# Kernel optimization log

Measured on AMD Instinct MI355X. Metric: run time of the kernel, lower is better.

Reference implementation:

```python
import jax, jax.numpy as jnp
import numpy as np

N, E, DIN, DOUT = 50000, 500000, 128, 128


def setup_inputs() -> dict:
    key = jax.random.key(0)
    ks = jax.random.split(key, 12)
    s = 0.02
    return {
        "x": jax.random.normal(ks[0], (N, DIN), jnp.float32),
        "pos": jax.random.normal(ks[1], (N, 3), jnp.float32),
        "edge_index": jax.random.randint(ks[2], (2, E), 0, N, jnp.int64),
        # mlp_h: Linear(DIN,DIN) -> ReLU -> Linear(DIN,3) -> Tanh
        "h_w1": jax.random.normal(ks[3], (DIN, DIN), jnp.float32) * s,
        "h_b1": jnp.zeros((DIN,), jnp.float32),
        "h_w2": jax.random.normal(ks[4], (DIN, 3), jnp.float32) * s,
        "h_b2": jnp.zeros((3,), jnp.float32),
        # mlp_f: Linear(DIN+3, DOUT) -> ReLU
        "f_w": jax.random.normal(ks[5], (DIN + 3, DOUT), jnp.float32) * s,
        "f_b": jnp.zeros((DOUT,), jnp.float32),
        # mlp_g: Linear(DOUT,DOUT) -> ReLU -> Linear(DOUT,DIN) -> ReLU
        "g_w1": jax.random.normal(ks[6], (DOUT, DOUT), jnp.float32) * s,
        "g_b1": jnp.zeros((DOUT,), jnp.float32),
        "g_w2": jax.random.normal(ks[7], (DOUT, DIN), jnp.float32) * s,
        "g_b2": jnp.zeros((DIN,), jnp.float32),
    }


def reference(x, pos, edge_index, h_w1, h_b1, h_w2, h_b2, f_w, f_b,
              g_w1, g_b1, g_w2, g_b2):
    # PointGNNConv (aggr='sum'):
    #   delta = mlp_h(x)                                   [N, 3]
    #   msg_e = mlp_f([pos_j - pos_i + delta_i, x_j])      [E, DOUT]
    #   agg_i = sum_{j in N(i)} msg_e                       [N, DOUT]
    #   out   = x + mlp_g(agg)                              [N, DIN]
    delta = jnp.tanh(jax.nn.relu(x @ h_w1 + h_b1) @ h_w2 + h_b2)
    src = edge_index[0]  # j (source)
    dst = edge_index[1]  # i (target)
    edge_feat = jnp.concatenate(
        [pos[src] - pos[dst] + delta[dst], x[src]], axis=-1)  # [E, DIN+3]
    msg = jax.nn.relu(edge_feat @ f_w + f_b)                   # [E, DOUT]
    agg = jax.ops.segment_sum(msg, dst, num_segments=N)        # [N, DOUT]
    out = jax.nn.relu(jax.nn.relu(agg @ g_w1 + g_b1) @ g_w2 + g_b2)
    return x + out
```

## Files before the change

### kernel.cpp

```cpp
#include <hip/hip_runtime.h>
#include <hip/hip_bf16.h>

typedef float f32x4 __attribute__((ext_vector_type(4)));
typedef short bf16x8 __attribute__((ext_vector_type(8)));
typedef unsigned short u16x8 __attribute__((ext_vector_type(8)));

#define MFMA16(a, b, c) __builtin_amdgcn_mfma_f32_16x16x32_bf16((a), (b), (c), 0, 0, 0)
#define BCAP 128

static __device__ __forceinline__ short f2bf(float f) {
    union { float f; unsigned u; } v; v.f = f;
    unsigned r = v.u + 0x7FFFu + ((v.u >> 16) & 1u);
    return (short)(r >> 16);
}
static __device__ __forceinline__ float bflo(unsigned u) {
    union { unsigned u; float f; } v; v.u = u << 16; return v.f;
}
static __device__ __forceinline__ float bfhi(unsigned u) {
    union { unsigned u; float f; } v; v.u = u & 0xffff0000u; return v.f;
}
static __device__ __forceinline__ unsigned packbf(float lo, float hi) {
    return ((unsigned)(unsigned short)f2bf(lo)) | (((unsigned)(unsigned short)f2bf(hi)) << 16);
}

__global__ __launch_bounds__(256) void k_prep(
    const float* __restrict__ hw1, const float* __restrict__ fw,
    const float* __restrict__ gw1, const float* __restrict__ gw2,
    unsigned short* __restrict__ wT,
    const int* __restrict__ ei, int* __restrict__ flag,
    int* __restrict__ cursor, int N)
{
    const int gtid = blockIdx.x * 256 + threadIdx.x;
    if (gtid == 0) {
        int nz = 0;
        for (int i = 0; i < 64; ++i) nz |= ei[2 * i + 1];
        *flag = (nz != 0) ? 1 : 0;
    }
    for (int i = gtid; i < N; i += 16384) cursor[i] = i << 7;
    const int idx = gtid;
    const int c = idx >> 7, k = idx & 127;
    wT[0 * 16384 + idx] = (unsigned short)f2bf(hw1[(size_t)k * 128 + c]);
    wT[1 * 16384 + idx] = (unsigned short)f2bf(fw[(size_t)(3 + k) * 128 + c]);
    wT[2 * 16384 + idx] = (unsigned short)f2bf(gw1[(size_t)k * 128 + c]);
    wT[3 * 16384 + idx] = (unsigned short)f2bf(gw2[(size_t)k * 128 + c]);
}

__global__ __launch_bounds__(256) void k_front(
    const float* __restrict__ x, const float* __restrict__ pos,
    const float* __restrict__ hb1,
    const float* __restrict__ hw2, const float* __restrict__ hb2,
    const float* __restrict__ fw, const float* __restrict__ fb,
    const unsigned short* __restrict__ wT,
    unsigned short* __restrict__ Pb, unsigned short* __restrict__ Qb, int N,
    const int* __restrict__ ei, int* __restrict__ cursor, int* __restrict__ list,
    const int* __restrict__ flag, int E)
{
    __shared__ float t1s[16][132];
    __shared__ unsigned short pls[16 * 128];
    __shared__ float poss[48];
    __shared__ float dqs[48];
    __shared__ float w2s[384];
    __shared__ float w3s[384];
    __shared__ float b1s[128], fbs[128], b2s[3];

    const int tid = threadIdx.x;
    const int lane = tid & 63, wave = tid >> 6;
    const int r16 = lane & 15, kg = lane >> 4;

    {
        const int f = *flag;
        const int stride2 = gridDim.x * 256 * 2;
        for (int e0 = (blockIdx.x * 256 + tid) * 2; e0 < E; e0 += stride2) {
            int s0, s1 = 0, d0, d1 = 0;
            const bool two = (e0 + 1 < E);
            if (f) {
                if (two) {
                    const int2 sv = *reinterpret_cast<const int2*>(ei + e0);
                    const int2 dv = *reinterpret_cast<const int2*>(ei + (size_t)E + e0);
                    s0 = sv.x; s1 = sv.y; d0 = dv.x; d1 = dv.y;
                } else { s0 = ei[e0]; d0 = ei[(size_t)E + e0]; }
            } else {
                if (two) {
                    const int4 sv = *reinterpret_cast<const int4*>(ei + 2 * (size_t)e0);
                    const int4 dv = *reinterpret_cast<const int4*>(ei + 2 * ((size_t)E + e0));
                    s0 = sv.x; s1 = sv.z; d0 = dv.x; d1 = dv.z;
                } else { s0 = ei[2 * (size_t)e0]; d0 = ei[2 * ((size_t)E + e0)]; }
            }
            int p = atomicAdd(&cursor[d0], 1);
            if (p < (d0 << 7) + BCAP) list[p] = s0;
            if (two) {
                p = atomicAdd(&cursor[d1], 1);
                if (p < (d1 << 7) + BCAP) list[p] = s1;
            }
        }
    }

    for (int i = tid; i < 128; i += 256) { b1s[i] = hb1[i]; fbs[i] = fb[i]; }
    for (int i = tid; i < 384; i += 256) { w2s[i] = hw2[i]; w3s[i] = fw[i]; }
    if (tid < 3) b2s[tid] = hb2[tid];

    const unsigned short* hw1T = wT;
    const unsigned short* fwxT = wT + 16384;
    bf16x8 bw1[2][4], bwx[2][4];
    #pragma unroll
    for (int si = 0; si < 2; ++si) {
        const int c = (wave * 2 + si) * 16 + r16;
        #pragma unroll
        for (int t = 0; t < 4; ++t) {
            const int k0 = t * 32 + kg * 8;
            bw1[si][t] = *reinterpret_cast<const bf16x8*>(hw1T + c * 128 + k0);
            bwx[si][t] = *reinterpret_cast<const bf16x8*>(fwxT + c * 128 + k0);
        }
    }

    const int ntiles = (N + 15) >> 4;
    int tile = blockIdx.x;

    float4 px[8];
    float posr = 0.f;
    if (tile < ntiles) {
        int arow = (tile << 4) + r16; if (arow >= N) arow = N - 1;
        const float4* p = reinterpret_cast<const float4*>(x + (size_t)arow * 128);
        #pragma unroll
        for (int t = 0; t < 4; ++t) { px[2 * t] = p[t * 8 + kg * 2]; px[2 * t + 1] = p[t * 8 + kg * 2 + 1]; }
        if (tid < 48) {
            int r = tid / 3, m = tid - 3 * r;
            int rr = (tile << 4) + r; if (rr >= N) rr = N - 1;
            posr = pos[(size_t)rr * 3 + m];
        }
    }
    __syncthreads();

    for (; tile < ntiles; tile += gridDim.x) {
        const int row0 = tile << 4;

        if (tid < 48) poss[tid] = posr;
        bf16x8 a[4];
        #pragma unroll
        for (int t = 0; t < 4; ++t) {
            float4 u0 = px[2 * t], u1 = px[2 * t + 1];
            bf16x8 v;
            v[0] = f2bf(u0.x); v[1] = f2bf(u0.y); v[2] = f2bf(u0.z); v[3] = f2bf(u0.w);
            v[4] = f2bf(u1.x); v[5] = f2bf(u1.y); v[6] = f2bf(u1.z); v[7] = f2bf(u1.w);
            a[t] = v;
        }
        const int ntile = tile + gridDim.x;
        if (ntile < ntiles) {
            int arow = (ntile << 4) + r16; if (arow >= N) arow = N - 1;
            const float4* p = reinterpret_cast<const float4*>(x + (size_t)arow * 128);
            #pragma unroll
            for (int t = 0; t < 4; ++t) { px[2 * t] = p[t * 8 + kg * 2]; px[2 * t + 1] = p[t * 8 + kg * 2 + 1]; }
            if (tid < 48) {
                int r = tid / 3, m = tid - 3 * r;
                int rr = (ntile << 4) + r; if (rr >= N) rr = N - 1;
                posr = pos[(size_t)rr * 3 + m];
            }
        }
        f32x4 acc1[2], accP[2];
        acc1[0] = 0.f; acc1[1] = 0.f; accP[0] = 0.f; accP[1] = 0.f;
        #pragma unroll
        for (int t = 0; t < 4; ++t) {
            #pragma unroll
            for (int si = 0; si < 2; ++si) {
                acc1[si] = MFMA16(a[t], bw1[si][t], acc1[si]);
                accP[si] = MFMA16(a[t], bwx[si][t], accP[si]);
            }
        }
        #pragma unroll
        for (int si = 0; si < 2; ++si) {
            const int c = (wave * 2 + si) * 16 + r16;
            #pragma unroll
            for (int j = 0; j < 4; ++j) {
                const int r = kg * 4 + j;
                t1s[r][c] = fmaxf(acc1[si][j] + b1s[c], 0.f);
            }
        }
        __syncthreads();

        #pragma unroll
        for (int si = 0; si < 2; ++si) {
            const int c = (wave * 2 + si) * 16 + r16;
            const int g = c >> 3, ce = c & 7;
            #pragma unroll
            for (int j = 0; j < 4; ++j) {
                const int r = kg * 4 + j;
                float pval = accP[si][j] + fbs[c]
                    + poss[r * 3 + 0] * w3s[0 * 128 + c]
                    + poss[r * 3 + 1] * w3s[1 * 128 + c]
                    + poss[r * 3 + 2] * w3s[2 * 128 + c];
                pls[r * 128 + (g ^ r) * 8 + ce] = (unsigned short)f2bf(pval);
            }
        }
        if (tid < 192) {
            const int pair = tid >> 2, h = tid & 3;
            const int r = pair / 3, m = pair - 3 * r;
            float s = 0.f;
            const int k0 = h * 32;
            #pragma unroll
            for (int k = k0; k < k0 + 32; k += 4) {
                float4 tv = *reinterpret_cast<const float4*>(&t1s[r][k]);
                s += tv.x * w2s[(k + 0) * 3 + m] + tv.y * w2s[(k + 1) * 3 + m]
                   + tv.z * w2s[(k + 2) * 3 + m] + tv.w * w2s[(k + 3) * 3 + m];
            }
            s += __shfl_xor(s, 1, 4);
            s += __shfl_xor(s, 2, 4);
            if (h == 0) dqs[pair] = tanhf(s + b2s[m]) - poss[pair];
        }
        __syncthreads();

        {
            const int row = tid >> 4, g0 = tid & 15;
            if (row0 + row < N) {
                u16x8 v = *reinterpret_cast<const u16x8*>(&pls[row * 128 + (g0 ^ row) * 8]);
                *reinterpret_cast<u16x8*>(Pb + (size_t)(row0 + row) * 128 + g0 * 8) = v;
            }
        }
        #pragma unroll
        for (int it = 0; it < 2; ++it) {
            const int idx = tid + it * 256;
            const int cg = idx & 31, r = idx >> 5;
            const int c0 = cg * 4;
            if (row0 + r < N) {
                const float d0 = dqs[r * 3 + 0], d1 = dqs[r * 3 + 1], d2 = dqs[r * 3 + 2];
                float q0 = d0 * w3s[c0 + 0] + d1 * w3s[128 + c0 + 0] + d2 * w3s[256 + c0 + 0];
                float q1 = d0 * w3s[c0 + 1] + d1 * w3s[128 + c0 + 1] + d2 * w3s[256 + c0 + 1];
                float q2 = d0 * w3s[c0 + 2] + d1 * w3s[128 + c0 + 2] + d2 * w3s[256 + c0 + 2];
                float q3 = d0 * w3s[c0 + 3] + d1 * w3s[128 + c0 + 3] + d2 * w3s[256 + c0 + 3];
                uint2 w; w.x = packbf(q0, q1); w.y = packbf(q2, q3);
                *reinterpret_cast<uint2*>(Qb + (size_t)(row0 + r) * 128 + c0) = w;
            }
        }
        __syncthreads();
    }
}

__global__ __launch_bounds__(256) void k_agg(
    const unsigned short* __restrict__ Pb, const unsigned short* __restrict__ Qb,
    const int* __restrict__ cursor, const int* __restrict__ list,
    unsigned short* __restrict__ aggb, int N)
{
    const int d = blockIdx.x * 16 + (threadIdx.x >> 4);
    if (d >= N) return;
    const int l = threadIdx.x & 15;
    const int start = d << 7;
    const int deg = min(cursor[d] - start, BCAP);

    const uint4 qu = *reinterpret_cast<const uint4*>(Qb + (size_t)d * 128 + l * 8);
    const float q0 = bflo(qu.x), q1 = bfhi(qu.x), q2 = bflo(qu.y), q3 = bfhi(qu.y);
    const float q4 = bflo(qu.z), q5 = bfhi(qu.z), q6 = bflo(qu.w), q7 = bfhi(qu.w);
    float a0 = 0.f, a1 = 0.f, a2 = 0.f, a3 = 0.f;
    float a4 = 0.f, a5 = 0.f, a6 = 0.f, a7 = 0.f;

#define ACC_EDGE(u) do { \
        a0 += fmaxf(bflo(u.x) + q0, 0.f); \
        a1 += fmaxf(bfhi(u.x) + q1, 0.f); \
        a2 += fmaxf(bflo(u.y) + q2, 0.f); \
        a3 += fmaxf(bfhi(u.y) + q3, 0.f); \
        a4 += fmaxf(bflo(u.z) + q4, 0.f); \
        a5 += fmaxf(bfhi(u.z) + q5, 0.f); \
        a6 += fmaxf(bflo(u.w) + q6, 0.f); \
        a7 += fmaxf(bfhi(u.w) + q7, 0.f); \
    } while (0)

    for (int b0 = 0; b0 < deg; b0 += 16) {
        int s = 0;
        if (b0 + l < deg) s = list[start + b0 + l];
        const int m = min(16, deg - b0);
        int k = 0;
        for (; k + 4 <= m; k += 4) {
            const int sj0 = __shfl(s, k + 0, 16);
            const int sj1 = __shfl(s, k + 1, 16);
            const int sj2 = __shfl(s, k + 2, 16);
            const int sj3 = __shfl(s, k + 3, 16);
            const uint4 u0 = *reinterpret_cast<const uint4*>(Pb + (size_t)sj0 * 128 + l * 8);
            const uint4 u1 = *reinterpret_cast<const uint4*>(Pb + (size_t)sj1 * 128 + l * 8);
            const uint4 u2 = *reinterpret_cast<const uint4*>(Pb + (size_t)sj2 * 128 + l * 8);
            const uint4 u3 = *reinterpret_cast<const uint4*>(Pb + (size_t)sj3 * 128 + l * 8);
            ACC_EDGE(u0); ACC_EDGE(u1); ACC_EDGE(u2); ACC_EDGE(u3);
        }
        for (; k < m; ++k) {
            const int sj = __shfl(s, k, 16);
            const uint4 u = *reinterpret_cast<const uint4*>(Pb + (size_t)sj * 128 + l * 8);
            ACC_EDGE(u);
        }
    }
#undef ACC_EDGE

    uint4 w;
    w.x = packbf(a0, a1); w.y = packbf(a2, a3);
    w.z = packbf(a4, a5); w.w = packbf(a6, a7);
    *reinterpret_cast<uint4*>(aggb + (size_t)d * 128 + l * 8) = w;
}

__global__ __launch_bounds__(256) void k_back(
    const unsigned short* __restrict__ aggb, const float* __restrict__ x,
    const unsigned short* __restrict__ wT,
    const float* __restrict__ gb1, const float* __restrict__ gb2,
    float* __restrict__ out, int N)
{
    __shared__ unsigned short uls[16 * 128];
    __shared__ float b1s[128], b2s[128];

    const int tid = threadIdx.x;
    const int lane = tid & 63, wave = tid >> 6;
    const int r16 = lane & 15, kg = lane >> 4;

    for (int i = tid; i < 128; i += 256) { b1s[i] = gb1[i]; b2s[i] = gb2[i]; }

    const unsigned short* gw1T = wT + 2 * 16384;
    const unsigned short* gw2T = wT + 3 * 16384;
    bf16x8 bg1[2][4], bg2[2][4];
    #pragma unroll
    for (int si = 0; si < 2; ++si) {
        const int c = (wave * 2 + si) * 16 + r16;
        #pragma unroll
        for (int t = 0; t < 4; ++t) {
            const int k0 = t * 32 + kg * 8;
            bg1[si][t] = *reinterpret_cast<const bf16x8*>(gw1T + c * 128 + k0);
            bg2[si][t] = *reinterpret_cast<const bf16x8*>(gw2T + c * 128 + k0);
        }
    }

    const int ntiles = (N + 15) >> 4;
    int tile = blockIdx.x;

    bf16x8 a[4];
    float xv[2][4];
    if (tile < ntiles) {
        int arow = (tile << 4) + r16; if (arow >= N) arow = N - 1;
        #pragma unroll
        for (int t = 0; t < 4; ++t)
            a[t] = *reinterpret_cast<const bf16x8*>(aggb + (size_t)arow * 128 + t * 32 + kg * 8);
        #pragma unroll
        for (int si = 0; si < 2; ++si) {
            const int c = (wave * 2 + si) * 16 + r16;
            #pragma unroll
            for (int j = 0; j < 4; ++j) {
                const int r = (tile << 4) + kg * 4 + j;
                xv[si][j] = (r < N) ? x[(size_t)r * 128 + c] : 0.f;
            }
        }
    }
    __syncthreads();

    for (; tile < ntiles; tile += gridDim.x) {
        const int row0 = tile << 4;

        f32x4 accU[2];
        accU[0] = 0.f; accU[1] = 0.f;
        #pragma unroll
        for (int t = 0; t < 4; ++t) {
            #pragma unroll
            for (int si = 0; si < 2; ++si)
                accU[si] = MFMA16(a[t], bg1[si][t], accU[si]);
        }

        const int ntile = tile + gridDim.x;
        float xvn[2][4];
        if (ntile < ntiles) {
            int arow = (ntile << 4) + r16; if (arow >= N) arow = N - 1;
            #pragma unroll
            for (int t = 0; t < 4; ++t)
                a[t] = *reinterpret_cast<const bf16x8*>(aggb + (size_t)arow * 128 + t * 32 + kg * 8);
            #pragma unroll
            for (int si = 0; si < 2; ++si) {
                const int c = (wave * 2 + si) * 16 + r16;
                #pragma unroll
                for (int j = 0; j < 4; ++j) {
                    const int r = (ntile << 4) + kg * 4 + j;
                    xvn[si][j] = (r < N) ? x[(size_t)r * 128 + c] : 0.f;
                }
            }
        }

        __syncthreads();
        #pragma unroll
        for (int si = 0; si < 2; ++si) {
            const int c = (wave * 2 + si) * 16 + r16;
            const int g = c >> 3, ce = c & 7;
            #pragma unroll
            for (int j = 0; j < 4; ++j) {
                const int r = kg * 4 + j;
                uls[r * 128 + (g ^ r) * 8 + ce] =
                    (unsigned short)f2bf(fmaxf(accU[si][j] + b1s[c], 0.f));
            }
        }
        __syncthreads();

        bf16x8 a2[4];
        #pragma unroll
        for (int t = 0; t < 4; ++t) {
            const int p = (t * 4 + kg) ^ r16;
            a2[t] = *reinterpret_cast<const bf16x8*>(&uls[r16 * 128 + p * 8]);
        }
        f32x4 accO[2];
        accO[0] = 0.f; accO[1] = 0.f;
        #pragma unroll
        for (int t = 0; t < 4; ++t) {
            #pragma unroll
            for (int si = 0; si < 2; ++si)
                accO[si] = MFMA16(a2[t], bg2[si][t], accO[si]);
        }
        #pragma unroll
        for (int si = 0; si < 2; ++si) {
            const int c = (wave * 2 + si) * 16 + r16;
            #pragma unroll
            for (int j = 0; j < 4; ++j) {
                const int r = kg * 4 + j;
                if (row0 + r < N) {
                    out[(size_t)(row0 + r) * 128 + c] =
                        xv[si][j] + fmaxf(accO[si][j] + b2s[c], 0.f);
                }
            }
        }
        if (ntile < ntiles) {
            #pragma unroll
            for (int si = 0; si < 2; ++si)
                #pragma unroll
                for (int j = 0; j < 4; ++j)
                    xv[si][j] = xvn[si][j];
        }
    }
}

extern "C" void kernel_launch(void* const* d_in, const int* in_sizes, int n_in,
                              void* d_out, int out_size, void* d_ws, size_t ws_size,
                              hipStream_t stream)
{
    const float* x   = (const float*)d_in[0];
    const float* pos = (const float*)d_in[1];
    const int*   ei  = (const int*)d_in[2];
    const float* hw1 = (const float*)d_in[3];
    const float* hb1 = (const float*)d_in[4];
    const float* hw2 = (const float*)d_in[5];
    const float* hb2 = (const float*)d_in[6];
    const float* fw  = (const float*)d_in[7];
    const float* fb  = (const float*)d_in[8];
    const float* gw1 = (const float*)d_in[9];
    const float* gb1 = (const float*)d_in[10];
    const float* gw2 = (const float*)d_in[11];
    const float* gb2 = (const float*)d_in[12];
    float* out = (float*)d_out;

    const int N = in_sizes[0] / 128;
    const int E = in_sizes[2] / 2;

    const size_t NW = (size_t)N * 128;
    unsigned short* Pb   = (unsigned short*)d_ws;
    unsigned short* Qb   = Pb + NW;
    unsigned short* aggb = Qb + NW;
    unsigned short* wT   = aggb + NW;
    int* cursor = (int*)(wT + 4 * 16384);
    int* list   = cursor + N;
    int* flag   = list + (size_t)N * BCAP;

    k_prep<<<64, 256, 0, stream>>>(hw1, fw, gw1, gw2, wT, ei, flag, cursor, N);
    k_front<<<1042, 256, 0, stream>>>(x, pos, hb1, hw2, hb2, fw, fb, wT, Pb, Qb, N,
                                      ei, cursor, list, flag, E);
    k_agg<<<(N + 15) / 16, 256, 0, stream>>>(Pb, Qb, cursor, list, aggb, N);
    k_back<<<1042, 256, 0, stream>>>(aggb, x, wT, gb1, gb2, out, N);
}
```

Before: 112.8 us.

## Move edge bucketing into prep kernel and deepen aggregation unroll

Edge bucketing (atomic cursor increments and list writes) moves out of the front MLP kernel into the prep kernel, which now launches 1024 blocks. The cursor becomes a relative count zeroed by a memset, and each thread recomputes the index-format flag locally, so the separate flag buffer is dropped. The aggregation loop gains an 8-wide gather unroll to keep more loads in flight. This adds a memset launch and makes the prep kernel heavier, but lets the front kernel run only the MLP work.

```diff
diff --git a/kernel.cpp b/kernel.cpp
--- a/kernel.cpp
+++ b/kernel.cpp
@@ -27,22 +27,49 @@
     const float* __restrict__ hw1, const float* __restrict__ fw,
     const float* __restrict__ gw1, const float* __restrict__ gw2,
     unsigned short* __restrict__ wT,
-    const int* __restrict__ ei, int* __restrict__ flag,
-    int* __restrict__ cursor, int N)
+    const int* __restrict__ ei, int* __restrict__ cursor,
+    int* __restrict__ list, int E)
 {
-    const int gtid = blockIdx.x * 256 + threadIdx.x;
-    if (gtid == 0) {
-        int nz = 0;
-        for (int i = 0; i < 64; ++i) nz |= ei[2 * i + 1];
-        *flag = (nz != 0) ? 1 : 0;
-    }
-    for (int i = gtid; i < N; i += 16384) cursor[i] = i << 7;
-    const int idx = gtid;
-    const int c = idx >> 7, k = idx & 127;
-    wT[0 * 16384 + idx] = (unsigned short)f2bf(hw1[(size_t)k * 128 + c]);
-    wT[1 * 16384 + idx] = (unsigned short)f2bf(fw[(size_t)(3 + k) * 128 + c]);
-    wT[2 * 16384 + idx] = (unsigned short)f2bf(gw1[(size_t)k * 128 + c]);
-    wT[3 * 16384 + idx] = (unsigned short)f2bf(gw2[(size_t)k * 128 + c]);
+    const int bid = blockIdx.x, tid = threadIdx.x;
+
+    if (bid < 64) {
+        const int idx = bid * 256 + tid;
+        const int c = idx >> 7, k = idx & 127;
+        wT[0 * 16384 + idx] = (unsigned short)f2bf(hw1[(size_t)k * 128 + c]);
+        wT[1 * 16384 + idx] = (unsigned short)f2bf(fw[(size_t)(3 + k) * 128 + c]);
+        wT[2 * 16384 + idx] = (unsigned short)f2bf(gw1[(size_t)k * 128 + c]);
+        wT[3 * 16384 + idx] = (unsigned short)f2bf(gw2[(size_t)k * 128 + c]);
+    }
+
+    int nz = 0;
+    #pragma unroll
+    for (int i = 0; i < 8; ++i) nz |= ei[2 * i + 1];
+    const int f = (nz != 0);
+
+    const int stride2 = gridDim.x * 256 * 2;
+    for (int e0 = (bid * 256 + tid) * 2; e0 < E; e0 += stride2) {
+        int s0, s1 = 0, d0, d1 = 0;
+        const bool two = (e0 + 1 < E);
+        if (f) {
+            if (two) {
+                const int2 sv = *reinterpret_cast<const int2*>(ei + e0);
+                const int2 dv = *reinterpret_cast<const int2*>(ei + (size_t)E + e0);
+                s0 = sv.x; s1 = sv.y; d0 = dv.x; d1 = dv.y;
+            } else { s0 = ei[e0]; d0 = ei[(size_t)E + e0]; }
+        } else {
+            if (two) {
+                const int4 sv = *reinterpret_cast<const int4*>(ei + 2 * (size_t)e0);
+                const int4 dv = *reinterpret_cast<const int4*>(ei + 2 * ((size_t)E + e0));
+                s0 = sv.x; s1 = sv.z; d0 = dv.x; d1 = dv.z;
+            } else { s0 = ei[2 * (size_t)e0]; d0 = ei[2 * ((size_t)E + e0)]; }
+        }
+        int p = atomicAdd(&cursor[d0], 1);
+        if (p < BCAP) list[((size_t)d0 << 7) + p] = s0;
+        if (two) {
+            p = atomicAdd(&cursor[d1], 1);
+            if (p < BCAP) list[((size_t)d1 << 7) + p] = s1;
+        }
+    }
 }
 
 __global__ __launch_bounds__(256) void k_front(
@@ -51,9 +78,7 @@
     const float* __restrict__ hw2, const float* __restrict__ hb2,
     const float* __restrict__ fw, const float* __restrict__ fb,
     const unsigned short* __restrict__ wT,
-    unsigned short* __restrict__ Pb, unsigned short* __restrict__ Qb, int N,
-    const int* __restrict__ ei, int* __restrict__ cursor, int* __restrict__ list,
-    const int* __restrict__ flag, int E)
+    unsigned short* __restrict__ Pb, unsigned short* __restrict__ Qb, int N)
 {
     __shared__ float t1s[16][132];
     __shared__ unsigned short pls[16 * 128];
@@ -66,34 +91,6 @@
     const int tid = threadIdx.x;
     const int lane = tid & 63, wave = tid >> 6;
     const int r16 = lane & 15, kg = lane >> 4;
-
-    {
-        const int f = *flag;
-        const int stride2 = gridDim.x * 256 * 2;
-        for (int e0 = (blockIdx.x * 256 + tid) * 2; e0 < E; e0 += stride2) {
-            int s0, s1 = 0, d0, d1 = 0;
-            const bool two = (e0 + 1 < E);
-            if (f) {
-                if (two) {
-                    const int2 sv = *reinterpret_cast<const int2*>(ei + e0);
-                    const int2 dv = *reinterpret_cast<const int2*>(ei + (size_t)E + e0);
-                    s0 = sv.x; s1 = sv.y; d0 = dv.x; d1 = dv.y;
-                } else { s0 = ei[e0]; d0 = ei[(size_t)E + e0]; }
-            } else {
-                if (two) {
-                    const int4 sv = *reinterpret_cast<const int4*>(ei + 2 * (size_t)e0);
-                    const int4 dv = *reinterpret_cast<const int4*>(ei + 2 * ((size_t)E + e0));
-                    s0 = sv.x; s1 = sv.z; d0 = dv.x; d1 = dv.z;
-                } else { s0 = ei[2 * (size_t)e0]; d0 = ei[2 * ((size_t)E + e0)]; }
-            }
-            int p = atomicAdd(&cursor[d0], 1);
-            if (p < (d0 << 7) + BCAP) list[p] = s0;
-            if (two) {
-                p = atomicAdd(&cursor[d1], 1);
-                if (p < (d1 << 7) + BCAP) list[p] = s1;
-            }
-        }
-    }
 
     for (int i = tid; i < 128; i += 256) { b1s[i] = hb1[i]; fbs[i] = fb[i]; }
     for (int i = tid; i < 384; i += 256) { w2s[i] = hw2[i]; w3s[i] = fw[i]; }
@@ -243,7 +240,7 @@
     if (d >= N) return;
     const int l = threadIdx.x & 15;
     const int start = d << 7;
-    const int deg = min(cursor[d] - start, BCAP);
+    const int deg = min(cursor[d], BCAP);
 
     const uint4 qu = *reinterpret_cast<const uint4*>(Qb + (size_t)d * 128 + l * 8);
     const float q0 = bflo(qu.x), q1 = bfhi(qu.x), q2 = bflo(qu.y), q3 = bfhi(qu.y);
@@ -267,6 +264,26 @@
         if (b0 + l < deg) s = list[start + b0 + l];
         const int m = min(16, deg - b0);
         int k = 0;
+        for (; k + 8 <= m; k += 8) {
+            const int sj0 = __shfl(s, k + 0, 16);
+            const int sj1 = __shfl(s, k + 1, 16);
+            const int sj2 = __shfl(s, k + 2, 16);
+            const int sj3 = __shfl(s, k + 3, 16);
+            const int sj4 = __shfl(s, k + 4, 16);
+            const int sj5 = __shfl(s, k + 5, 16);
+            const int sj6 = __shfl(s, k + 6, 16);
+            const int sj7 = __shfl(s, k + 7, 16);
+            const uint4 u0 = *reinterpret_cast<const uint4*>(Pb + (size_t)sj0 * 128 + l * 8);
+            const uint4 u1 = *reinterpret_cast<const uint4*>(Pb + (size_t)sj1 * 128 + l * 8);
+            const uint4 u2 = *reinterpret_cast<const uint4*>(Pb + (size_t)sj2 * 128 + l * 8);
+            const uint4 u3 = *reinterpret_cast<const uint4*>(Pb + (size_t)sj3 * 128 + l * 8);
+            const uint4 u4 = *reinterpret_cast<const uint4*>(Pb + (size_t)sj4 * 128 + l * 8);
+            const uint4 u5 = *reinterpret_cast<const uint4*>(Pb + (size_t)sj5 * 128 + l * 8);
+            const uint4 u6 = *reinterpret_cast<const uint4*>(Pb + (size_t)sj6 * 128 + l * 8);
+            const uint4 u7 = *reinterpret_cast<const uint4*>(Pb + (size_t)sj7 * 128 + l * 8);
+            ACC_EDGE(u0); ACC_EDGE(u1); ACC_EDGE(u2); ACC_EDGE(u3);
+            ACC_EDGE(u4); ACC_EDGE(u5); ACC_EDGE(u6); ACC_EDGE(u7);
+        }
         for (; k + 4 <= m; k += 4) {
             const int sj0 = __shfl(s, k + 0, 16);
             const int sj1 = __shfl(s, k + 1, 16);
@@ -452,11 +469,10 @@
     unsigned short* wT   = aggb + NW;
     int* cursor = (int*)(wT + 4 * 16384);
     int* list   = cursor + N;
-    int* flag   = list + (size_t)N * BCAP;
-
-    k_prep<<<64, 256, 0, stream>>>(hw1, fw, gw1, gw2, wT, ei, flag, cursor, N);
-    k_front<<<1042, 256, 0, stream>>>(x, pos, hb1, hw2, hb2, fw, fb, wT, Pb, Qb, N,
-                                      ei, cursor, list, flag, E);
+
+    hipMemsetAsync(cursor, 0, (size_t)N * sizeof(int), stream);
+    k_prep<<<1024, 256, 0, stream>>>(hw1, fw, gw1, gw2, wT, ei, cursor, list, E);
+    k_front<<<1042, 256, 0, stream>>>(x, pos, hb1, hw2, hb2, fw, fb, wT, Pb, Qb, N);
     k_agg<<<(N + 15) / 16, 256, 0, stream>>>(Pb, Qb, cursor, list, aggb, N);
     k_back<<<1042, 256, 0, stream>>>(aggb, x, wT, gb1, gb2, out, N);
 }
```

Result: slower. 121.9 us (+8.0%).

## Split edge scatter across blocks before/after node tiles; widen gather unroll to 8

Applied to the files above, without the earlier changes.

The edge-to-bucket scatter in k_front is moved into a helper. Odd blocks run it before their node-tile MLP work and even blocks run it after, so the atomic-heavy scatter overlaps with the compute-heavy dense phase instead of every block doing it up front. Each block still scatters the same edges as before. k_agg also gains an 8-wide unrolled gather loop ahead of the 4-wide one, putting more independent loads in flight at the cost of extra registers.

```diff
diff --git a/kernel.cpp b/kernel.cpp
--- a/kernel.cpp
+++ b/kernel.cpp
@@ -43,6 +43,36 @@
     wT[1 * 16384 + idx] = (unsigned short)f2bf(fw[(size_t)(3 + k) * 128 + c]);
     wT[2 * 16384 + idx] = (unsigned short)f2bf(gw1[(size_t)k * 128 + c]);
     wT[3 * 16384 + idx] = (unsigned short)f2bf(gw2[(size_t)k * 128 + c]);
+}
+
+static __device__ __forceinline__ void scatter_edges(
+    const int* __restrict__ ei, int* __restrict__ cursor, int* __restrict__ list,
+    int f, int E, int gbase, int gstride)
+{
+    const int stride2 = gstride * 2;
+    for (int e0 = gbase * 2; e0 < E; e0 += stride2) {
+        int s0, s1 = 0, d0, d1 = 0;
+        const bool two = (e0 + 1 < E);
+        if (f) {
+            if (two) {
+                const int2 sv = *reinterpret_cast<const int2*>(ei + e0);
+                const int2 dv = *reinterpret_cast<const int2*>(ei + (size_t)E + e0);
+                s0 = sv.x; s1 = sv.y; d0 = dv.x; d1 = dv.y;
+            } else { s0 = ei[e0]; d0 = ei[(size_t)E + e0]; }
+        } else {
+            if (two) {
+                const int4 sv = *reinterpret_cast<const int4*>(ei + 2 * (size_t)e0);
+                const int4 dv = *reinterpret_cast<const int4*>(ei + 2 * ((size_t)E + e0));
+                s0 = sv.x; s1 = sv.z; d0 = dv.x; d1 = dv.z;
+            } else { s0 = ei[2 * (size_t)e0]; d0 = ei[2 * ((size_t)E + e0)]; }
+        }
+        int p = atomicAdd(&cursor[d0], 1);
+        if (p < (d0 << 7) + BCAP) list[p] = s0;
+        if (two) {
+            p = atomicAdd(&cursor[d1], 1);
+            if (p < (d1 << 7) + BCAP) list[p] = s1;
+        }
+    }
 }
 
 __global__ __launch_bounds__(256) void k_front(
@@ -66,34 +96,8 @@
     const int tid = threadIdx.x;
     const int lane = tid & 63, wave = tid >> 6;
     const int r16 = lane & 15, kg = lane >> 4;
-
-    {
-        const int f = *flag;
-        const int stride2 = gridDim.x * 256 * 2;
-        for (int e0 = (blockIdx.x * 256 + tid) * 2; e0 < E; e0 += stride2) {
-            int s0, s1 = 0, d0, d1 = 0;
-            const bool two = (e0 + 1 < E);
-            if (f) {
-                if (two) {
-                    const int2 sv = *reinterpret_cast<const int2*>(ei + e0);
-                    const int2 dv = *reinterpret_cast<const int2*>(ei + (size_t)E + e0);
-                    s0 = sv.x; s1 = sv.y; d0 = dv.x; d1 = dv.y;
-                } else { s0 = ei[e0]; d0 = ei[(size_t)E + e0]; }
-            } else {
-                if (two) {
-                    const int4 sv = *reinterpret_cast<const int4*>(ei + 2 * (size_t)e0);
-                    const int4 dv = *reinterpret_cast<const int4*>(ei + 2 * ((size_t)E + e0));
-                    s0 = sv.x; s1 = sv.z; d0 = dv.x; d1 = dv.z;
-                } else { s0 = ei[2 * (size_t)e0]; d0 = ei[2 * ((size_t)E + e0)]; }
-            }
-            int p = atomicAdd(&cursor[d0], 1);
-            if (p < (d0 << 7) + BCAP) list[p] = s0;
-            if (two) {
-                p = atomicAdd(&cursor[d1], 1);
-                if (p < (d1 << 7) + BCAP) list[p] = s1;
-            }
-        }
-    }
+    const int f = *flag;
+    const bool early = (blockIdx.x & 1);
 
     for (int i = tid; i < 128; i += 256) { b1s[i] = hb1[i]; fbs[i] = fb[i]; }
     for (int i = tid; i < 384; i += 256) { w2s[i] = hw2[i]; w3s[i] = fw[i]; }
@@ -129,6 +133,10 @@
             posr = pos[(size_t)rr * 3 + m];
         }
     }
+
+    if (early)
+        scatter_edges(ei, cursor, list, f, E, blockIdx.x * 256 + tid, gridDim.x * 256);
+
     __syncthreads();
 
     for (; tile < ntiles; tile += gridDim.x) {
@@ -232,6 +240,9 @@
         }
         __syncthreads();
     }
+
+    if (!early)
+        scatter_edges(ei, cursor, list, f, E, blockIdx.x * 256 + tid, gridDim.x * 256);
 }
 
 __global__ __launch_bounds__(256) void k_agg(
@@ -267,6 +278,26 @@
         if (b0 + l < deg) s = list[start + b0 + l];
         const int m = min(16, deg - b0);
         int k = 0;
+        for (; k + 8 <= m; k += 8) {
+            const int sj0 = __shfl(s, k + 0, 16);
+            const int sj1 = __shfl(s, k + 1, 16);
+            const int sj2 = __shfl(s, k + 2, 16);
+            const int sj3 = __shfl(s, k + 3, 16);
+            const int sj4 = __shfl(s, k + 4, 16);
+            const int sj5 = __shfl(s, k + 5, 16);
+            const int sj6 = __shfl(s, k + 6, 16);
+            const int sj7 = __shfl(s, k + 7, 16);
+            const uint4 u0 = *reinterpret_cast<const uint4*>(Pb + (size_t)sj0 * 128 + l * 8);
+            const uint4 u1 = *reinterpret_cast<const uint4*>(Pb + (size_t)sj1 * 128 + l * 8);
+            const uint4 u2 = *reinterpret_cast<const uint4*>(Pb + (size_t)sj2 * 128 + l * 8);
+            const uint4 u3 = *reinterpret_cast<const uint4*>(Pb + (size_t)sj3 * 128 + l * 8);
+            const uint4 u4 = *reinterpret_cast<const uint4*>(Pb + (size_t)sj4 * 128 + l * 8);
+            const uint4 u5 = *reinterpret_cast<const uint4*>(Pb + (size_t)sj5 * 128 + l * 8);
+            const uint4 u6 = *reinterpret_cast<const uint4*>(Pb + (size_t)sj6 * 128 + l * 8);
+            const uint4 u7 = *reinterpret_cast<const uint4*>(Pb + (size_t)sj7 * 128 + l * 8);
+            ACC_EDGE(u0); ACC_EDGE(u1); ACC_EDGE(u2); ACC_EDGE(u3);
+            ACC_EDGE(u4); ACC_EDGE(u5); ACC_EDGE(u6); ACC_EDGE(u7);
+        }
         for (; k + 4 <= m; k += 4) {
             const int sj0 = __shfl(s, k + 0, 16);
             const int sj1 = __shfl(s, k + 1, 16);
```

New measurement: 102.5 us. 9.1% less time.
